# Optimization experiments

Measured on AMD Instinct MI355X. Metric: run time of the kernel, lower is better.

The kernel has to match this reference:

```python
import jax, jax.numpy as jnp
import numpy as np

B, T, C, H = 2, 2048, 1024, 16  # batch, seq, n_embd, n_head


def setup_inputs() -> dict:
    key = jax.random.key(0)
    k1, k2, k3 = jax.random.split(key, 3)
    scale = 0.02
    return {
        "x": jax.random.normal(k1, (B, T, C), dtype=jnp.float32),
        "W_attn": jax.random.normal(k2, (3 * C, C), dtype=jnp.float32) * scale,
        "b_attn": jnp.zeros((3 * C,), dtype=jnp.float32),
        "W_proj": jax.random.normal(k3, (C, C), dtype=jnp.float32) * scale,
        "b_proj": jnp.zeros((C,), dtype=jnp.float32),
        "alpha": jnp.asarray(1.0, dtype=jnp.float32),
        "beta": jnp.asarray(0.1, dtype=jnp.float32),
        "gamma": jnp.asarray(0.1, dtype=jnp.float32),
    }


def reference(x, W_attn, b_attn, W_proj, b_proj, alpha, beta, gamma):
    Bx, Tx, Cx = x.shape
    d = Cx // H  # head dim
    qkv = x @ W_attn.T + b_attn                      # [B,T,3C]
    q, k, v = jnp.split(qkv, 3, axis=-1)

    def to_heads(t):
        return t.reshape(Bx, Tx, H, d).transpose(0, 2, 1, 3)  # [B,H,T,d]

    q, k, v = to_heads(q), to_heads(k), to_heads(v)

    inv_sqrt_d = jnp.asarray(1.0 / np.sqrt(d), dtype=x.dtype)
    scores = jnp.einsum('bhtd,bhsd->bhts', q, k) * inv_sqrt_d  # [B,H,T,T]

    causal = jnp.tril(jnp.ones((Tx, Tx), dtype=bool))
    scores = jnp.where(causal, scores, -jnp.inf)
    att = jax.nn.softmax(scores, axis=-1)

    # Id buffer = softmax(10000*eye) == identity; MC buffer = softmax(10000*tril)
    # == uniform causal prefix average: MC[i, j<=i] = 1/(i+1).
    id_m = jnp.eye(Tx, dtype=x.dtype)
    mc = causal.astype(x.dtype) / jnp.arange(1, Tx + 1, dtype=x.dtype)[:, None]

    shaped = beta * att + alpha * id_m - gamma * mc  # dropout p=0 -> identity
    y = jnp.einsum('bhts,bhsd->bhtd', shaped, v)     # [B,H,T,d]
    y = y.transpose(0, 2, 1, 3).reshape(Bx, Tx, Cx)
    return y @ W_proj.T + b_proj
```

## Files before the change

kernel.cpp:

```cpp
#include <hip/hip_runtime.h>
#include <stdint.h>

#define Bsz  2
#define Tseq 2048
#define Cemb 1024
#define NH   16
#define HD   64

typedef __attribute__((ext_vector_type(8))) __bf16 bf16x8;
typedef __attribute__((ext_vector_type(4))) float  f32x4;
typedef __attribute__((ext_vector_type(8))) unsigned short u16x8;

#define MFMA16(a, b, c) __builtin_amdgcn_mfma_f32_16x16x32_bf16((a), (b), (c), 0, 0, 0)

__device__ __forceinline__ unsigned short f2bf(float f) {
  union { float f; unsigned int u; } v; v.f = f;
  unsigned int u = v.u;
  u += 0x7fffu + ((u >> 16) & 1u);
  return (unsigned short)(u >> 16);
}
__device__ __forceinline__ float bf2f(unsigned short h) {
  union { unsigned int u; float f; } v; v.u = ((unsigned int)h) << 16;
  return v.f;
}
__device__ __forceinline__ unsigned int pack_bf2(float a, float b) {
  union { float f; unsigned int u; } va, vb; va.f = a; vb.f = b;
  return __builtin_amdgcn_perm(vb.u + 0x8000u, va.u + 0x8000u, 0x07060302u);
}

typedef __attribute__((address_space(1))) const unsigned int GU;
typedef __attribute__((address_space(3))) unsigned int LU;
__device__ __forceinline__ void load_lds16(const void* g, void* l) {
  __builtin_amdgcn_global_load_lds((GU*)g, (LU*)l, 16, 0, 0);
}

#define XE  4194304
#define WAE 3145728
__global__ void cast3_kernel(const float* __restrict__ x,
                             const float* __restrict__ wa,
                             const float* __restrict__ wp,
                             unsigned short* __restrict__ out) {
  const int i = (blockIdx.x * blockDim.x + threadIdx.x) * 4;
  const float* src;
  int off;
  if (i < XE) { src = x; off = i; }
  else if (i < XE + WAE) { src = wa; off = i - XE; }
  else { src = wp; off = i - (XE + WAE); }
  const float4 f = *(const float4*)(src + off);
  ushort4 o;
  o.x = f2bf(f.x); o.y = f2bf(f.y); o.z = f2bf(f.z); o.w = f2bf(f.w);
  *(ushort4*)(out + i) = o;
}

__global__ __launch_bounds__(256) void gemm_qkv_kernel(
    const unsigned short* __restrict__ A,
    const unsigned short* __restrict__ Bw,
    const float* __restrict__ bias,
    unsigned short* __restrict__ qkv,
    unsigned short* __restrict__ vt) {
  const int K = Cemb;
  __shared__ unsigned short sA[128 * 32];
  __shared__ unsigned short sB[128 * 32];
  const int tid = threadIdx.x;
  const int wave = tid >> 6, lane = tid & 63;
  const int quad = lane >> 4, lrow = lane & 15;
  const int l7 = lrow & 7;
  const int wm = (wave >> 1) * 64, wn = (wave & 1) * 64;
  const int tileM = blockIdx.y * 128, tileN = blockIdx.x * 128;

  f32x4 acc[4][4];
#pragma unroll
  for (int i = 0; i < 4; ++i)
#pragma unroll
    for (int j = 0; j < 4; ++j) acc[i][j] = (f32x4){0.f, 0.f, 0.f, 0.f};

  for (int k0 = 0; k0 < K; k0 += 32) {
    __syncthreads();
#pragma unroll
    for (int s = 0; s < 2; ++s) {
      const int cid = tid + s * 256;
      const int r = cid >> 2, ko = (cid & 3) * 8;
      load_lds16(&A[(size_t)(tileM + r) * K + k0 + ko], &sA[cid * 8]);
      load_lds16(&Bw[(size_t)(tileN + r) * K + k0 + ko], &sB[cid * 8]);
    }
    __syncthreads();
    bf16x8 af[4], bfm[4];
#pragma unroll
    for (int mt = 0; mt < 4; ++mt)
      af[mt] = *(const bf16x8*)&sA[(wm + mt * 16 + lrow) * 32 + quad * 8];
#pragma unroll
    for (int nt = 0; nt < 4; ++nt)
      bfm[nt] = *(const bf16x8*)&sB[(wn + nt * 16 + lrow) * 32 + quad * 8];
#pragma unroll
    for (int mt = 0; mt < 4; ++mt)
#pragma unroll
      for (int nt = 0; nt < 4; ++nt)
        acc[mt][nt] = MFMA16(af[mt], bfm[nt], acc[mt][nt]);
  }

  __syncthreads();
  unsigned short* sEp = sA + wave * 1024;
  float bias_v[4];
#pragma unroll
  for (int nt = 0; nt < 4; ++nt) bias_v[nt] = bias[tileN + wn + nt * 16 + lrow];
  const int gn0 = tileN + wn;
  const int part = gn0 >> 10, h = (gn0 & 1023) >> 6;
  const float qscl = (part == 0) ? 0.125f : 1.0f;

#pragma unroll
  for (int mt = 0; mt < 4; ++mt) {
#pragma unroll
    for (int nt = 0; nt < 4; ++nt)
#pragma unroll
      for (int reg = 0; reg < 4; ++reg) {
        const int q = quad * 4 + reg;
        const int ch = (nt * 2 + (lrow >> 3)) ^ (q & 7);
        sEp[q * 64 + ch * 8 + l7] = f2bf((acc[mt][nt][reg] + bias_v[nt]) * qscl);
      }
    __builtin_amdgcn_wave_barrier();
#pragma unroll
    for (int i = 0; i < 2; ++i) {
      const int c = i * 64 + lane;
      const int r = c >> 3, ch2 = c & 7;
      const u16x8 row = *(const u16x8*)&sEp[r * 64 + ((ch2 ^ (r & 7)) << 3)];
      const int gm = tileM + wm + mt * 16 + r;
      const int bb = gm >> 11, t = gm & 2047;
      *(u16x8*)&qkv[((((size_t)part * Bsz + bb) * NH + h) * Tseq + t) * HD + ch2 * 8] = row;
    }
    if (part == 2) {
      unsigned int w[8];
#pragma unroll
      for (int q = 0; q < 16; q += 2) {
        const unsigned short a0 =
            sEp[q * 64 + (((lane >> 3) ^ (q & 7)) << 3) + (lane & 7)];
        const unsigned short a1 =
            sEp[(q + 1) * 64 + (((lane >> 3) ^ ((q + 1) & 7)) << 3) + (lane & 7)];
        w[q >> 1] = (unsigned int)a0 | ((unsigned int)a1 << 16);
      }
      const int gm0 = tileM + wm + mt * 16;
      const int bb = gm0 >> 11, t0 = gm0 & 2047;
      unsigned short* dst = &vt[(((size_t)bb * NH + h) * HD + lane) * Tseq + t0];
      *(uint4*)(dst) = *(const uint4*)&w[0];
      *(uint4*)(dst + 8) = *(const uint4*)&w[4];
    }
    __builtin_amdgcn_wave_barrier();
  }
}

__global__ __launch_bounds__(256) void gemm_proj_kernel(
    const unsigned short* __restrict__ A,
    const unsigned short* __restrict__ Bw,
    const float* __restrict__ bias,
    float* __restrict__ out) {
  const int K = Cemb;
  __shared__ unsigned short sA[32 * 32];
  __shared__ unsigned short sB[128 * 32];
  const int tid = threadIdx.x;
  const int wave = tid >> 6, lane = tid & 63;
  const int quad = lane >> 4, lrow = lane & 15;
  const int wn = wave * 32;
  const int tileM = blockIdx.y * 32, tileN = blockIdx.x * 128;

  f32x4 acc[2][2];
#pragma unroll
  for (int i = 0; i < 2; ++i)
#pragma unroll
    for (int j = 0; j < 2; ++j) acc[i][j] = (f32x4){0.f, 0.f, 0.f, 0.f};

  for (int k0 = 0; k0 < K; k0 += 32) {
    __syncthreads();
    if (tid < 128) {
      const int r = tid >> 2, ko = (tid & 3) * 8;
      load_lds16(&A[(size_t)(tileM + r) * K + k0 + ko], &sA[tid * 8]);
    }
#pragma unroll
    for (int s = 0; s < 2; ++s) {
      const int cB = tid + s * 256;
      const int rB = cB >> 2, koB = (cB & 3) * 8;
      load_lds16(&Bw[(size_t)(tileN + rB) * K + k0 + koB], &sB[cB * 8]);
    }
    __syncthreads();
    bf16x8 af[2], bfm[2];
#pragma unroll
    for (int mt = 0; mt < 2; ++mt)
      af[mt] = *(const bf16x8*)&sA[(mt * 16 + lrow) * 32 + quad * 8];
#pragma unroll
    for (int nt = 0; nt < 2; ++nt)
      bfm[nt] = *(const bf16x8*)&sB[(wn + nt * 16 + lrow) * 32 + quad * 8];
#pragma unroll
    for (int mt = 0; mt < 2; ++mt)
#pragma unroll
      for (int nt = 0; nt < 2; ++nt)
        acc[mt][nt] = MFMA16(af[mt], bfm[nt], acc[mt][nt]);
  }

#pragma unroll
  for (int mt = 0; mt < 2; ++mt)
#pragma unroll
    for (int nt = 0; nt < 2; ++nt)
#pragma unroll
      for (int reg = 0; reg < 4; ++reg) {
        const int gm = tileM + mt * 16 + quad * 4 + reg;
        const int gn = tileN + wn + nt * 16 + lrow;
        out[(size_t)gm * Cemb + gn] = acc[mt][nt][reg] + bias[gn];
      }
}

__global__ __launch_bounds__(256) void attn_kernel(
    const unsigned short* __restrict__ qkv,
    const unsigned short* __restrict__ vt,
    const float* __restrict__ palpha, const float* __restrict__ pbeta,
    const float* __restrict__ pgamma,
    unsigned short* __restrict__ y) {
  __shared__ unsigned short sK[2][64 * 64];
  __shared__ unsigned short sVt[2][64 * 64];

  const int tid = threadIdx.x;
  const int wave = tid >> 6, lane = tid & 63;
  const int quad = lane >> 4, lrow = lane & 15;
  const int bh = blockIdx.y;
  const int b = bh >> 4, h = bh & 15;

  const size_t partStride = (size_t)Bsz * NH * Tseq * HD;
  const size_t headoff = (size_t)bh * Tseq * HD;
  const unsigned short* Q = qkv + headoff;
  const unsigned short* Kp = qkv + partStride + headoff;
  const unsigned short* Vp = qkv + 2 * partStride + headoff;
  const unsigned short* Vt_g = vt + (size_t)bh * HD * Tseq;

  const float alpha = palpha[0], beta = pbeta[0], gamma = pgamma[0];

  union { unsigned short u[8]; bf16x8 v; } onesU;
#pragma unroll
  for (int j = 0; j < 8; ++j) onesU.u[j] = 0x3F80;
  const bf16x8 onesF = onesU.v;

  const int qtA = blockIdx.x;
  const int qtB = 31 - qtA;
  const int q0A = qtA * 64, q0B = qtB * 64;

  const int qrowA = q0A + wave * 16 + lrow;
  const int qrowB = q0B + wave * 16 + lrow;
  const bf16x8 bQA0 = *(const bf16x8*)&Q[(size_t)qrowA * HD + quad * 8];
  const bf16x8 bQA1 = *(const bf16x8*)&Q[(size_t)qrowA * HD + 32 + quad * 8];
  const bf16x8 bQB0 = *(const bf16x8*)&Q[(size_t)qrowB * HD + quad * 8];
  const bf16x8 bQB1 = *(const bf16x8*)&Q[(size_t)qrowB * HD + 32 + quad * 8];

  const int prow = ((lrow & 12) << 1) | (lrow & 3);

  f32x4 OtA[4], UtA[4], LA, OtB[4], UtB[4], LB;
#pragma unroll
  for (int dt = 0; dt < 4; ++dt) {
    OtA[dt] = (f32x4){0.f, 0.f, 0.f, 0.f};
    UtA[dt] = (f32x4){0.f, 0.f, 0.f, 0.f};
    OtB[dt] = (f32x4){0.f, 0.f, 0.f, 0.f};
    UtB[dt] = (f32x4){0.f, 0.f, 0.f, 0.f};
  }
  LA = (f32x4){0.f, 0.f, 0.f, 0.f};
  LB = (f32x4){0.f, 0.f, 0.f, 0.f};

  auto stage_tile = [&](int it, int buf) {
    const int j0 = it * 64;
#pragma unroll
    for (int s = 0; s < 2; ++s) {
      const int c = tid + s * 256;
      const int r = c >> 3, cc = c & 7;
      const int pk = cc ^ (r & 7) ^ ((r & 16) >> 2);
      load_lds16(&Kp[(size_t)(j0 + r) * HD + pk * 8], &sK[buf][c * 8]);
      load_lds16(&Vt_g[(size_t)r * Tseq + j0 + pk * 8], &sVt[buf][c * 8]);
    }
  };

  stage_tile(0, 0);

  const int ntiles = qtB + 1;
  for (int it = 0; it < ntiles; ++it) {
    const int cur = it & 1;
    __syncthreads();
    if (it + 1 < ntiles) stage_tile(it + 1, (it + 1) & 1);

    const unsigned short* K_ = sK[cur];
    const unsigned short* Vt_ = sVt[cur];
    const int j0 = it * 64;
    const bool actA = (it <= qtA);
    const bool diagA = (it == qtA), diagB = (it == qtB);

    unsigned int pkA[4][2], pkB[4][2];
#pragma unroll
    for (int ct = 0; ct < 4; ++ct) {
      const int srow = (ct >> 1) * 32 + (ct & 1) * 4 + prow;
      const int hs = (srow & 7) ^ ((srow & 16) >> 2);
      const bf16x8 a0 = *(const bf16x8*)&K_[srow * 64 + ((quad ^ hs) << 3)];
      const bf16x8 a1 = *(const bf16x8*)&K_[srow * 64 + (((4 + quad) ^ hs) << 3)];
      const int sbase = j0 + (ct >> 1) * 32 + (ct & 1) * 4 + quad * 8;

      f32x4 sB = (f32x4){0.f, 0.f, 0.f, 0.f};
      sB = MFMA16(a0, bQB0, sB);
      sB = MFMA16(a1, bQB1, sB);
      float pB[4];
      if (diagB) {
#pragma unroll
        for (int reg = 0; reg < 4; ++reg)
          pB[reg] = __expf((sbase + reg > qrowB) ? -1e30f : sB[reg]);
      } else {
#pragma unroll
        for (int reg = 0; reg < 4; ++reg) pB[reg] = __expf(sB[reg]);
      }
      pkB[ct][0] = pack_bf2(pB[0], pB[1]);
      pkB[ct][1] = pack_bf2(pB[2], pB[3]);

      if (actA) {
        f32x4 sA = (f32x4){0.f, 0.f, 0.f, 0.f};
        sA = MFMA16(a0, bQA0, sA);
        sA = MFMA16(a1, bQA1, sA);
        float pA[4];
        if (diagA) {
#pragma unroll
          for (int reg = 0; reg < 4; ++reg)
            pA[reg] = __expf((sbase + reg > qrowA) ? -1e30f : sA[reg]);
        } else {
#pragma unroll
          for (int reg = 0; reg < 4; ++reg) pA[reg] = __expf(sA[reg]);
        }
        pkA[ct][0] = pack_bf2(pA[0], pA[1]);
        pkA[ct][1] = pack_bf2(pA[2], pA[3]);
      }
    }

    union { unsigned int w[4]; bf16x8 v; } tu;
    tu.w[0] = pkB[0][0]; tu.w[1] = pkB[0][1]; tu.w[2] = pkB[1][0]; tu.w[3] = pkB[1][1];
    const bf16x8 P1B = tu.v;
    tu.w[0] = pkB[2][0]; tu.w[1] = pkB[2][1]; tu.w[2] = pkB[3][0]; tu.w[3] = pkB[3][1];
    const bf16x8 P2B = tu.v;
    bf16x8 P1A = onesF, P2A = onesF;
    if (actA) {
      tu.w[0] = pkA[0][0]; tu.w[1] = pkA[0][1]; tu.w[2] = pkA[1][0]; tu.w[3] = pkA[1][1];
      P1A = tu.v;
      tu.w[0] = pkA[2][0]; tu.w[1] = pkA[2][1]; tu.w[2] = pkA[3][0]; tu.w[3] = pkA[3][1];
      P2A = tu.v;
    }

    LB = MFMA16(onesF, P1B, LB);
    LB = MFMA16(onesF, P2B, LB);
    if (actA) {
      LA = MFMA16(onesF, P1A, LA);
      LA = MFMA16(onesF, P2A, LA);
    }

    bf16x8 u1B = onesF, u2B = onesF, u1A = onesF, u2A = onesF;
    if (diagB) {
      union { unsigned short u[8]; bf16x8 v; } m0, m1;
#pragma unroll
      for (int jj = 0; jj < 8; ++jj) {
        m0.u[jj] = (j0 + quad * 8 + jj) <= qrowB ? (unsigned short)0x3F80 : (unsigned short)0;
        m1.u[jj] = (j0 + 32 + quad * 8 + jj) <= qrowB ? (unsigned short)0x3F80 : (unsigned short)0;
      }
      u1B = m0.v; u2B = m1.v;
    }
    if (actA && diagA) {
      union { unsigned short u[8]; bf16x8 v; } m0, m1;
#pragma unroll
      for (int jj = 0; jj < 8; ++jj) {
        m0.u[jj] = (j0 + quad * 8 + jj) <= qrowA ? (unsigned short)0x3F80 : (unsigned short)0;
        m1.u[jj] = (j0 + 32 + quad * 8 + jj) <= qrowA ? (unsigned short)0x3F80 : (unsigned short)0;
      }
      u1A = m0.v; u2A = m1.v;
    }

#pragma unroll
    for (int dt = 0; dt < 4; ++dt) {
      const int vr = dt * 16 + lrow;
      const int hvr = (vr & 7) ^ ((vr & 16) >> 2);
      const bf16x8 av0 = *(const bf16x8*)&Vt_[vr * 64 + ((quad ^ hvr) << 3)];
      const bf16x8 av1 = *(const bf16x8*)&Vt_[vr * 64 + (((4 + quad) ^ hvr) << 3)];
      OtB[dt] = MFMA16(av0, P1B, OtB[dt]);
      OtB[dt] = MFMA16(av1, P2B, OtB[dt]);
      UtB[dt] = MFMA16(av0, u1B, UtB[dt]);
      UtB[dt] = MFMA16(av1, u2B, UtB[dt]);
      if (actA) {
        OtA[dt] = MFMA16(av0, P1A, OtA[dt]);
        OtA[dt] = MFMA16(av1, P2A, OtA[dt]);
        UtA[dt] = MFMA16(av0, u1A, UtA[dt]);
        UtA[dt] = MFMA16(av1, u2A, UtA[dt]);
      }
    }
  }

  auto epilogue = [&](const f32x4* Ot, const f32x4* Ut, const f32x4& L, int qrow) {
    const float bl = beta / L[0];
    const float gi = gamma / (float)(qrow + 1);
    const size_t ybase = ((size_t)b * Tseq + qrow) * Cemb + h * HD;
#pragma unroll
    for (int dt = 0; dt < 4; ++dt) {
      const int d0 = dt * 16 + quad * 4;
      const ushort4 vv4 = *(const ushort4*)&Vp[(size_t)qrow * HD + d0];
      const unsigned short vu[4] = {vv4.x, vv4.y, vv4.z, vv4.w};
      ushort4 o;
      unsigned short* op = (unsigned short*)&o;
#pragma unroll
      for (int reg = 0; reg < 4; ++reg) {
        const float yv = bl * Ot[dt][reg] + alpha * bf2f(vu[reg]) - gi * Ut[dt][reg];
        op[reg] = f2bf(yv);
      }
      *(ushort4*)&y[ybase + d0] = o;
    }
  };
  epilogue(OtA, UtA, LA, qrowA);
  epilogue(OtB, UtB, LB, qrowB);
}

extern "C" void kernel_launch(void* const* d_in, const int* in_sizes, int n_in,
                              void* d_out, int out_size, void* d_ws, size_t ws_size,
                              hipStream_t stream) {
  const float* x  = (const float*)d_in[0];
  const float* Wa = (const float*)d_in[1];
  const float* ba = (const float*)d_in[2];
  const float* Wp = (const float*)d_in[3];
  const float* bp = (const float*)d_in[4];
  const float* alpha = (const float*)d_in[5];
  const float* beta  = (const float*)d_in[6];
  const float* gamma = (const float*)d_in[7];
  float* out = (float*)d_out;

  unsigned short* ws = (unsigned short*)d_ws;
  unsigned short* xb   = ws;
  unsigned short* wab  = xb + (size_t)XE;
  unsigned short* wpb  = wab + (size_t)WAE;
  unsigned short* qkvb = wpb + (size_t)1024 * 1024;
  unsigned short* yb   = qkvb + (size_t)3 * Bsz * NH * Tseq * HD;
  unsigned short* vtb  = yb + (size_t)Bsz * Tseq * Cemb;

  cast3_kernel<<<(XE + WAE + 1048576) / 4 / 256, 256, 0, stream>>>(x, Wa, Wp, xb);

  gemm_qkv_kernel<<<dim3(3072 / 128, 4096 / 128), 256, 0, stream>>>(xb, wab, ba, qkvb, vtb);
  attn_kernel<<<dim3(16, Bsz * NH), 256, 0, stream>>>(qkvb, vtb, alpha, beta, gamma, yb);
  gemm_proj_kernel<<<dim3(1024 / 128, 4096 / 32), 256, 0, stream>>>(yb, wpb, bp, out);
}
```

Measured before the change: 197.7 us.

## Split KV tiles across two wave groups per attention block with LDS reduction

Doubles the attention block to 512 threads. Two groups of four waves process alternating KV tiles, each with its own double-buffered K/V staging. After the loop, partial output, uniform-average and denominator accumulators from the second group are reduced into the first through shared memory before the epilogue. This halves the serial tile chain per block and raises wave count per CU. In exchange it adds LDS usage, extra barriers and a reduction step.

New measurement: 201.3 us. About the same (+1.8%).

```diff
diff --git a/kernel.cpp b/kernel.cpp
--- a/kernel.cpp
+++ b/kernel.cpp
@@ -206,20 +206,26 @@
       }
 }
 
-__global__ __launch_bounds__(256) void attn_kernel(
+__global__ __launch_bounds__(512) void attn_kernel(
     const unsigned short* __restrict__ qkv,
     const unsigned short* __restrict__ vt,
     const float* __restrict__ palpha, const float* __restrict__ pbeta,
     const float* __restrict__ pgamma,
     unsigned short* __restrict__ y) {
-  __shared__ unsigned short sK[2][64 * 64];
-  __shared__ unsigned short sVt[2][64 * 64];
+  __shared__ __align__(16) unsigned short SM[32768];
 
   const int tid = threadIdx.x;
   const int wave = tid >> 6, lane = tid & 63;
+  const int grp = wave >> 2, wq = wave & 3;
+  const int gtid = tid & 255;
   const int quad = lane >> 4, lrow = lane & 15;
   const int bh = blockIdx.y;
   const int b = bh >> 4, h = bh & 15;
+
+  unsigned short* sK0 = SM + (grp * 2 + 0) * 4096;
+  unsigned short* sK1 = SM + (grp * 2 + 1) * 4096;
+  unsigned short* sV0 = SM + 16384 + (grp * 2 + 0) * 4096;
+  unsigned short* sV1 = SM + 16384 + (grp * 2 + 1) * 4096;
 
   const size_t partStride = (size_t)Bsz * NH * Tseq * HD;
   const size_t headoff = (size_t)bh * Tseq * HD;
@@ -239,8 +245,8 @@
   const int qtB = 31 - qtA;
   const int q0A = qtA * 64, q0B = qtB * 64;
 
-  const int qrowA = q0A + wave * 16 + lrow;
-  const int qrowB = q0B + wave * 16 + lrow;
+  const int qrowA = q0A + wq * 16 + lrow;
+  const int qrowB = q0B + wq * 16 + lrow;
   const bf16x8 bQA0 = *(const bf16x8*)&Q[(size_t)qrowA * HD + quad * 8];
   const bf16x8 bQA1 = *(const bf16x8*)&Q[(size_t)qrowA * HD + 32 + quad * 8];
   const bf16x8 bQB0 = *(const bf16x8*)&Q[(size_t)qrowB * HD + quad * 8];
@@ -259,31 +265,33 @@
   LA = (f32x4){0.f, 0.f, 0.f, 0.f};
   LB = (f32x4){0.f, 0.f, 0.f, 0.f};
 
-  auto stage_tile = [&](int it, int buf) {
-    const int j0 = it * 64;
+  auto stage_tile = [&](int t, unsigned short* Kb, unsigned short* Vb) {
+    const int j0 = t * 64;
 #pragma unroll
     for (int s = 0; s < 2; ++s) {
-      const int c = tid + s * 256;
+      const int c = gtid + s * 256;
       const int r = c >> 3, cc = c & 7;
       const int pk = cc ^ (r & 7) ^ ((r & 16) >> 2);
-      load_lds16(&Kp[(size_t)(j0 + r) * HD + pk * 8], &sK[buf][c * 8]);
-      load_lds16(&Vt_g[(size_t)r * Tseq + j0 + pk * 8], &sVt[buf][c * 8]);
+      load_lds16(&Kp[(size_t)(j0 + r) * HD + pk * 8], &Kb[c * 8]);
+      load_lds16(&Vt_g[(size_t)r * Tseq + j0 + pk * 8], &Vb[c * 8]);
     }
   };
 
-  stage_tile(0, 0);
-
-  const int ntiles = qtB + 1;
-  for (int it = 0; it < ntiles; ++it) {
-    const int cur = it & 1;
+  stage_tile(grp, sK0, sV0);
+
+  const int NI = (qtB >> 1) + 1;
+  for (int i = 0; i < NI; ++i) {
     __syncthreads();
-    if (it + 1 < ntiles) stage_tile(it + 1, (it + 1) & 1);
-
-    const unsigned short* K_ = sK[cur];
-    const unsigned short* Vt_ = sVt[cur];
-    const int j0 = it * 64;
-    const bool actA = (it <= qtA);
-    const bool diagA = (it == qtA), diagB = (it == qtB);
+    const int t = 2 * i + grp;
+    const int tn = t + 2;
+    if (tn <= qtB) stage_tile(tn, (i & 1) ? sK0 : sK1, (i & 1) ? sV0 : sV1);
+    if (t > qtB) continue;
+
+    const unsigned short* K_ = (i & 1) ? sK1 : sK0;
+    const unsigned short* Vt_ = (i & 1) ? sV1 : sV0;
+    const int j0 = t * 64;
+    const bool actA = (t <= qtA);
+    const bool diagA = (t == qtA), diagB = (t == qtB);
 
     unsigned int pkA[4][2], pkB[4][2];
 #pragma unroll
@@ -386,27 +394,74 @@
     }
   }
 
-  auto epilogue = [&](const f32x4* Ot, const f32x4* Ut, const f32x4& L, int qrow) {
-    const float bl = beta / L[0];
-    const float gi = gamma / (float)(qrow + 1);
-    const size_t ybase = ((size_t)b * Tseq + qrow) * Cemb + h * HD;
-#pragma unroll
-    for (int dt = 0; dt < 4; ++dt) {
-      const int d0 = dt * 16 + quad * 4;
-      const ushort4 vv4 = *(const ushort4*)&Vp[(size_t)qrow * HD + d0];
-      const unsigned short vu[4] = {vv4.x, vv4.y, vv4.z, vv4.w};
-      ushort4 o;
-      unsigned short* op = (unsigned short*)&o;
-#pragma unroll
-      for (int reg = 0; reg < 4; ++reg) {
-        const float yv = bl * Ot[dt][reg] + alpha * bf2f(vu[reg]) - gi * Ut[dt][reg];
-        op[reg] = f2bf(yv);
-      }
-      *(ushort4*)&y[ybase + d0] = o;
-    }
-  };
-  epilogue(OtA, UtA, LA, qrowA);
-  epilogue(OtB, UtB, LB, qrowB);
+  float* P = (float*)SM;
+  const int base = wq * 33 * 64 + lane;
+  __syncthreads();
+  if (grp == 1) {
+#pragma unroll
+    for (int dt = 0; dt < 4; ++dt)
+#pragma unroll
+      for (int reg = 0; reg < 4; ++reg) {
+        P[base + (dt * 4 + reg) * 64] = OtB[dt][reg];
+        P[base + (16 + dt * 4 + reg) * 64] = UtB[dt][reg];
+      }
+    P[base + 32 * 64] = LB[0];
+  }
+  __syncthreads();
+  if (grp == 0) {
+#pragma unroll
+    for (int dt = 0; dt < 4; ++dt)
+#pragma unroll
+      for (int reg = 0; reg < 4; ++reg) {
+        OtB[dt][reg] += P[base + (dt * 4 + reg) * 64];
+        UtB[dt][reg] += P[base + (16 + dt * 4 + reg) * 64];
+      }
+    LB[0] += P[base + 32 * 64];
+  }
+  __syncthreads();
+  if (grp == 1) {
+#pragma unroll
+    for (int dt = 0; dt < 4; ++dt)
+#pragma unroll
+      for (int reg = 0; reg < 4; ++reg) {
+        P[base + (dt * 4 + reg) * 64] = OtA[dt][reg];
+        P[base + (16 + dt * 4 + reg) * 64] = UtA[dt][reg];
+      }
+    P[base + 32 * 64] = LA[0];
+  }
+  __syncthreads();
+  if (grp == 0) {
+#pragma unroll
+    for (int dt = 0; dt < 4; ++dt)
+#pragma unroll
+      for (int reg = 0; reg < 4; ++reg) {
+        OtA[dt][reg] += P[base + (dt * 4 + reg) * 64];
+        UtA[dt][reg] += P[base + (16 + dt * 4 + reg) * 64];
+      }
+    LA[0] += P[base + 32 * 64];
+
+    auto epilogue = [&](const f32x4* Ot, const f32x4* Ut, float L, int qrow) {
+      const float bl = beta / L;
+      const float gi = gamma / (float)(qrow + 1);
+      const size_t ybase = ((size_t)b * Tseq + qrow) * Cemb + h * HD;
+#pragma unroll
+      for (int dt = 0; dt < 4; ++dt) {
+        const int d0 = dt * 16 + quad * 4;
+        const ushort4 vv4 = *(const ushort4*)&Vp[(size_t)qrow * HD + d0];
+        const unsigned short vu[4] = {vv4.x, vv4.y, vv4.z, vv4.w};
+        ushort4 o;
+        unsigned short* op = (unsigned short*)&o;
+#pragma unroll
+        for (int reg = 0; reg < 4; ++reg) {
+          const float yv = bl * Ot[dt][reg] + alpha * bf2f(vu[reg]) - gi * Ut[dt][reg];
+          op[reg] = f2bf(yv);
+        }
+        *(ushort4*)&y[ybase + d0] = o;
+      }
+    };
+    epilogue(OtA, UtA, LA[0], qrowA);
+    epilogue(OtB, UtB, LB[0], qrowB);
+  }
 }
 
 extern "C" void kernel_launch(void* const* d_in, const int* in_sizes, int n_in,
@@ -433,6 +488,6 @@
   cast3_kernel<<<(XE + WAE + 1048576) / 4 / 256, 256, 0, stream>>>(x, Wa, Wp, xb);
 
   gemm_qkv_kernel<<<dim3(3072 / 128, 4096 / 128), 256, 0, stream>>>(xb, wab, ba, qkvb, vtb);
-  attn_kernel<<<dim3(16, Bsz * NH), 256, 0, stream>>>(qkvb, vtb, alpha, beta, gamma, yb);
+  attn_kernel<<<dim3(16, Bsz * NH), 512, 0, stream>>>(qkvb, vtb, alpha, beta, gamma, yb);
   gemm_proj_kernel<<<dim3(1024 / 128, 4096 / 32), 256, 0, stream>>>(yb, wpb, bp, out);
 }
```

## Replace paired causal query tiles with one tile per block, heavy-first order

Applied to the files above, without the earlier changes.

The attention kernel no longer pairs query tile i with tile 31-i inside one block. Each block now handles a single 64-row query tile, and the grid doubles to 32 blocks per head, with the longest tiles scheduled first. This cuts the accumulator registers per thread, which can raise occupancy, and gives more blocks for load balancing. In exchange, K/V tiles staged in LDS are no longer shared between two query tiles, so K/V loads from global memory go up.

Result: slower. 203.8 us (+3.1%).

```diff
diff --git a/kernel.cpp b/kernel.cpp
--- a/kernel.cpp
+++ b/kernel.cpp
@@ -235,29 +235,22 @@
   for (int j = 0; j < 8; ++j) onesU.u[j] = 0x3F80;
   const bf16x8 onesF = onesU.v;
 
-  const int qtA = blockIdx.x;
-  const int qtB = 31 - qtA;
-  const int q0A = qtA * 64, q0B = qtB * 64;
-
-  const int qrowA = q0A + wave * 16 + lrow;
-  const int qrowB = q0B + wave * 16 + lrow;
-  const bf16x8 bQA0 = *(const bf16x8*)&Q[(size_t)qrowA * HD + quad * 8];
-  const bf16x8 bQA1 = *(const bf16x8*)&Q[(size_t)qrowA * HD + 32 + quad * 8];
-  const bf16x8 bQB0 = *(const bf16x8*)&Q[(size_t)qrowB * HD + quad * 8];
-  const bf16x8 bQB1 = *(const bf16x8*)&Q[(size_t)qrowB * HD + 32 + quad * 8];
+  const int qt = 31 - (int)blockIdx.x;
+  const int q0 = qt * 64;
+
+  const int qrow = q0 + wave * 16 + lrow;
+  const bf16x8 bQ0 = *(const bf16x8*)&Q[(size_t)qrow * HD + quad * 8];
+  const bf16x8 bQ1 = *(const bf16x8*)&Q[(size_t)qrow * HD + 32 + quad * 8];
 
   const int prow = ((lrow & 12) << 1) | (lrow & 3);
 
-  f32x4 OtA[4], UtA[4], LA, OtB[4], UtB[4], LB;
+  f32x4 Ot[4], Ut[4], L;
 #pragma unroll
   for (int dt = 0; dt < 4; ++dt) {
-    OtA[dt] = (f32x4){0.f, 0.f, 0.f, 0.f};
-    UtA[dt] = (f32x4){0.f, 0.f, 0.f, 0.f};
-    OtB[dt] = (f32x4){0.f, 0.f, 0.f, 0.f};
-    UtB[dt] = (f32x4){0.f, 0.f, 0.f, 0.f};
-  }
-  LA = (f32x4){0.f, 0.f, 0.f, 0.f};
-  LB = (f32x4){0.f, 0.f, 0.f, 0.f};
+    Ot[dt] = (f32x4){0.f, 0.f, 0.f, 0.f};
+    Ut[dt] = (f32x4){0.f, 0.f, 0.f, 0.f};
+  }
+  L = (f32x4){0.f, 0.f, 0.f, 0.f};
 
   auto stage_tile = [&](int it, int buf) {
     const int j0 = it * 64;
@@ -273,7 +266,7 @@
 
   stage_tile(0, 0);
 
-  const int ntiles = qtB + 1;
+  const int ntiles = qt + 1;
   for (int it = 0; it < ntiles; ++it) {
     const int cur = it & 1;
     __syncthreads();
@@ -282,89 +275,49 @@
     const unsigned short* K_ = sK[cur];
     const unsigned short* Vt_ = sVt[cur];
     const int j0 = it * 64;
-    const bool actA = (it <= qtA);
-    const bool diagA = (it == qtA), diagB = (it == qtB);
-
-    unsigned int pkA[4][2], pkB[4][2];
+    const bool diag = (it == qt);
+
+    unsigned int pk2[4][2];
 #pragma unroll
     for (int ct = 0; ct < 4; ++ct) {
       const int srow = (ct >> 1) * 32 + (ct & 1) * 4 + prow;
       const int hs = (srow & 7) ^ ((srow & 16) >> 2);
       const bf16x8 a0 = *(const bf16x8*)&K_[srow * 64 + ((quad ^ hs) << 3)];
       const bf16x8 a1 = *(const bf16x8*)&K_[srow * 64 + (((4 + quad) ^ hs) << 3)];
-      const int sbase = j0 + (ct >> 1) * 32 + (ct & 1) * 4 + quad * 8;
-
-      f32x4 sB = (f32x4){0.f, 0.f, 0.f, 0.f};
-      sB = MFMA16(a0, bQB0, sB);
-      sB = MFMA16(a1, bQB1, sB);
-      float pB[4];
-      if (diagB) {
+      f32x4 s = (f32x4){0.f, 0.f, 0.f, 0.f};
+      s = MFMA16(a0, bQ0, s);
+      s = MFMA16(a1, bQ1, s);
+      float p[4];
+      if (diag) {
+        const int sbase = j0 + (ct >> 1) * 32 + (ct & 1) * 4 + quad * 8;
 #pragma unroll
         for (int reg = 0; reg < 4; ++reg)
-          pB[reg] = __expf((sbase + reg > qrowB) ? -1e30f : sB[reg]);
+          p[reg] = __expf((sbase + reg > qrow) ? -1e30f : s[reg]);
       } else {
 #pragma unroll
-        for (int reg = 0; reg < 4; ++reg) pB[reg] = __expf(sB[reg]);
-      }
-      pkB[ct][0] = pack_bf2(pB[0], pB[1]);
-      pkB[ct][1] = pack_bf2(pB[2], pB[3]);
-
-      if (actA) {
-        f32x4 sA = (f32x4){0.f, 0.f, 0.f, 0.f};
-        sA = MFMA16(a0, bQA0, sA);
-        sA = MFMA16(a1, bQA1, sA);
-        float pA[4];
-        if (diagA) {
-#pragma unroll
-          for (int reg = 0; reg < 4; ++reg)
-            pA[reg] = __expf((sbase + reg > qrowA) ? -1e30f : sA[reg]);
-        } else {
-#pragma unroll
-          for (int reg = 0; reg < 4; ++reg) pA[reg] = __expf(sA[reg]);
-        }
-        pkA[ct][0] = pack_bf2(pA[0], pA[1]);
-        pkA[ct][1] = pack_bf2(pA[2], pA[3]);
-      }
-    }
-
+        for (int reg = 0; reg < 4; ++reg) p[reg] = __expf(s[reg]);
+      }
+      pk2[ct][0] = pack_bf2(p[0], p[1]);
+      pk2[ct][1] = pack_bf2(p[2], p[3]);
+    }
     union { unsigned int w[4]; bf16x8 v; } tu;
-    tu.w[0] = pkB[0][0]; tu.w[1] = pkB[0][1]; tu.w[2] = pkB[1][0]; tu.w[3] = pkB[1][1];
-    const bf16x8 P1B = tu.v;
-    tu.w[0] = pkB[2][0]; tu.w[1] = pkB[2][1]; tu.w[2] = pkB[3][0]; tu.w[3] = pkB[3][1];
-    const bf16x8 P2B = tu.v;
-    bf16x8 P1A = onesF, P2A = onesF;
-    if (actA) {
-      tu.w[0] = pkA[0][0]; tu.w[1] = pkA[0][1]; tu.w[2] = pkA[1][0]; tu.w[3] = pkA[1][1];
-      P1A = tu.v;
-      tu.w[0] = pkA[2][0]; tu.w[1] = pkA[2][1]; tu.w[2] = pkA[3][0]; tu.w[3] = pkA[3][1];
-      P2A = tu.v;
-    }
-
-    LB = MFMA16(onesF, P1B, LB);
-    LB = MFMA16(onesF, P2B, LB);
-    if (actA) {
-      LA = MFMA16(onesF, P1A, LA);
-      LA = MFMA16(onesF, P2A, LA);
-    }
-
-    bf16x8 u1B = onesF, u2B = onesF, u1A = onesF, u2A = onesF;
-    if (diagB) {
+    tu.w[0] = pk2[0][0]; tu.w[1] = pk2[0][1]; tu.w[2] = pk2[1][0]; tu.w[3] = pk2[1][1];
+    const bf16x8 P1 = tu.v;
+    tu.w[0] = pk2[2][0]; tu.w[1] = pk2[2][1]; tu.w[2] = pk2[3][0]; tu.w[3] = pk2[3][1];
+    const bf16x8 P2 = tu.v;
+
+    L = MFMA16(onesF, P1, L);
+    L = MFMA16(onesF, P2, L);
+
+    bf16x8 u1 = onesF, u2 = onesF;
+    if (diag) {
       union { unsigned short u[8]; bf16x8 v; } m0, m1;
 #pragma unroll
       for (int jj = 0; jj < 8; ++jj) {
-        m0.u[jj] = (j0 + quad * 8 + jj) <= qrowB ? (unsigned short)0x3F80 : (unsigned short)0;
-        m1.u[jj] = (j0 + 32 + quad * 8 + jj) <= qrowB ? (unsigned short)0x3F80 : (unsigned short)0;
-      }
-      u1B = m0.v; u2B = m1.v;
-    }
-    if (actA && diagA) {
-      union { unsigned short u[8]; bf16x8 v; } m0, m1;
-#pragma unroll
-      for (int jj = 0; jj < 8; ++jj) {
-        m0.u[jj] = (j0 + quad * 8 + jj) <= qrowA ? (unsigned short)0x3F80 : (unsigned short)0;
-        m1.u[jj] = (j0 + 32 + quad * 8 + jj) <= qrowA ? (unsigned short)0x3F80 : (unsigned short)0;
-      }
-      u1A = m0.v; u2A = m1.v;
+        m0.u[jj] = (j0 + quad * 8 + jj) <= qrow ? (unsigned short)0x3F80 : (unsigned short)0;
+        m1.u[jj] = (j0 + 32 + quad * 8 + jj) <= qrow ? (unsigned short)0x3F80 : (unsigned short)0;
+      }
+      u1 = m0.v; u2 = m1.v;
     }
 
 #pragma unroll
@@ -373,40 +326,30 @@
       const int hvr = (vr & 7) ^ ((vr & 16) >> 2);
       const bf16x8 av0 = *(const bf16x8*)&Vt_[vr * 64 + ((quad ^ hvr) << 3)];
       const bf16x8 av1 = *(const bf16x8*)&Vt_[vr * 64 + (((4 + quad) ^ hvr) << 3)];
-      OtB[dt] = MFMA16(av0, P1B, OtB[dt]);
-      OtB[dt] = MFMA16(av1, P2B, OtB[dt]);
-      UtB[dt] = MFMA16(av0, u1B, UtB[dt]);
-      UtB[dt] = MFMA16(av1, u2B, UtB[dt]);
-      if (actA) {
-        OtA[dt] = MFMA16(av0, P1A, OtA[dt]);
-        OtA[dt] = MFMA16(av1, P2A, OtA[dt]);
-        UtA[dt] = MFMA16(av0, u1A, UtA[dt]);
-        UtA[dt] = MFMA16(av1, u2A, UtA[dt]);
-      }
-    }
-  }
-
-  auto epilogue = [&](const f32x4* Ot, const f32x4* Ut, const f32x4& L, int qrow) {
-    const float bl = beta / L[0];
-    const float gi = gamma / (float)(qrow + 1);
-    const size_t ybase = ((size_t)b * Tseq + qrow) * Cemb + h * HD;
-#pragma unroll
-    for (int dt = 0; dt < 4; ++dt) {
-      const int d0 = dt * 16 + quad * 4;
-      const ushort4 vv4 = *(const ushort4*)&Vp[(size_t)qrow * HD + d0];
-      const unsigned short vu[4] = {vv4.x, vv4.y, vv4.z, vv4.w};
-      ushort4 o;
-      unsigned short* op = (unsigned short*)&o;
-#pragma unroll
-      for (int reg = 0; reg < 4; ++reg) {
-        const float yv = bl * Ot[dt][reg] + alpha * bf2f(vu[reg]) - gi * Ut[dt][reg];
-        op[reg] = f2bf(yv);
-      }
-      *(ushort4*)&y[ybase + d0] = o;
-    }
-  };
-  epilogue(OtA, UtA, LA, qrowA);
-  epilogue(OtB, UtB, LB, qrowB);
+      Ot[dt] = MFMA16(av0, P1, Ot[dt]);
+      Ot[dt] = MFMA16(av1, P2, Ot[dt]);
+      Ut[dt] = MFMA16(av0, u1, Ut[dt]);
+      Ut[dt] = MFMA16(av1, u2, Ut[dt]);
+    }
+  }
+
+  const float bl = beta / L[0];
+  const float gi = gamma / (float)(qrow + 1);
+  const size_t ybase = ((size_t)b * Tseq + qrow) * Cemb + h * HD;
+#pragma unroll
+  for (int dt = 0; dt < 4; ++dt) {
+    const int d0 = dt * 16 + quad * 4;
+    const ushort4 vv4 = *(const ushort4*)&Vp[(size_t)qrow * HD + d0];
+    const unsigned short vu[4] = {vv4.x, vv4.y, vv4.z, vv4.w};
+    ushort4 o;
+    unsigned short* op = (unsigned short*)&o;
+#pragma unroll
+    for (int reg = 0; reg < 4; ++reg) {
+      const float yv = bl * Ot[dt][reg] + alpha * bf2f(vu[reg]) - gi * Ut[dt][reg];
+      op[reg] = f2bf(yv);
+    }
+    *(ushort4*)&y[ybase + d0] = o;
+  }
 }
 
 extern "C" void kernel_launch(void* const* d_in, const int* in_sizes, int n_in,
@@ -433,6 +376,6 @@
   cast3_kernel<<<(XE + WAE + 1048576) / 4 / 256, 256, 0, stream>>>(x, Wa, Wp, xb);
 
   gemm_qkv_kernel<<<dim3(3072 / 128, 4096 / 128), 256, 0, stream>>>(xb, wab, ba, qkvb, vtb);
-  attn_kernel<<<dim3(16, Bsz * NH), 256, 0, stream>>>(qkvb, vtb, alpha, beta, gamma, yb);
+  attn_kernel<<<dim3(32, Bsz * NH), 256, 0, stream>>>(qkvb, vtb, alpha, beta, gamma, yb);
   gemm_proj_kernel<<<dim3(1024 / 128, 4096 / 32), 256, 0, stream>>>(yb, wpb, bp, out);
 }
```
